# Optimization experiments

Measured on AMD Instinct MI355X. Metric: run time of the kernel, lower is better.

## Reference

```python
import jax, jax.numpy as jnp
import numpy as np

N, E = 50000, 800000
F_IN, F_EMB1, F_EMB2, F_HID, F_OUT = 128, 512, 128, 1024, 64


def _linear_params(k, fan_in, fan_out):
    s = 1.0 / np.sqrt(fan_in)
    kw, kb = jax.random.split(k)
    W = jax.random.uniform(kw, (fan_in, fan_out), jnp.float32, -s, s)
    b = jax.random.uniform(kb, (fan_out,), jnp.float32, -s, s)
    return W, b


def setup_inputs() -> dict:
    key = jax.random.key(0)
    ks = jax.random.split(key, 8)
    x = jax.random.normal(ks[0], (N, F_IN), jnp.float32)
    src = jax.random.randint(ks[1], (E,), 0, N)
    dst = jax.random.randint(ks[2], (E,), 0, N)
    edge_index = jnp.stack([src, dst])  # [2, E]
    edge_weight = jax.random.uniform(ks[3], (E,), jnp.float32)  # positive weights
    W1, b1 = _linear_params(ks[4], F_IN, F_EMB1)
    W2, b2 = _linear_params(ks[5], F_EMB1, F_EMB2)
    W3, b3 = _linear_params(ks[6], F_EMB2, F_HID)
    W4, b4 = _linear_params(ks[7], F_HID, F_OUT)
    return dict(x=x, edge_index=edge_index, edge_weight=edge_weight,
                W1=W1, b1=b1, W2=W2, b2=b2, W3=W3, b3=b3, W4=W4, b4=b4)


def gcn_conv(x, src, dst, w, W, b):
    """PyG GCNConv: transform, then sym-normalized weighted aggregation with self-loops.
    out = D^{-1/2} (A_w + I) D^{-1/2} (x W) + b,  deg = scatter(w @ dst) + 1."""
    n = x.shape[0]
    h = x @ W  # [N, F_out]
    deg = jax.ops.segment_sum(w, dst, num_segments=n) + 1.0  # +1 for self-loop weight
    dinv = jax.lax.rsqrt(deg)
    norm = dinv[src] * w * dinv[dst]  # [E]
    agg = jax.ops.segment_sum(norm[:, None] * h[src], dst, num_segments=n)
    agg = agg + h / deg[:, None]  # self-loop: dinv[i]*1*dinv[i] * h[i]
    return agg + b


def reference(x, edge_index, edge_weight, W1, b1, W2, b2, W3, b3, W4, b4):
    src, dst = edge_index[0], edge_index[1]
    h = jax.nn.relu(gcn_conv(x, src, dst, edge_weight, W1, b1))
    # graph_normalization=False -> identity; dropout is identity in eval mode
    h = jax.nn.relu(gcn_conv(h, src, dst, edge_weight, W2, b2))
    h = jax.nn.relu(h @ W3 + b3)
    out = jax.nn.relu(h @ W4 + b4)
    return out
```

## Files before the change

### kernel.cpp

```cpp
#include <hip/hip_runtime.h>


#define ELLW 64
#define C64S 16

typedef short bf16x8 __attribute__((ext_vector_type(8)));
typedef float f32x4 __attribute__((ext_vector_type(4)));

__device__ __forceinline__ unsigned short f2b(float f) {
    unsigned u = __builtin_bit_cast(unsigned, f);
    unsigned r = (u + 0x7FFFu + ((u >> 16) & 1u)) >> 16;
    return (unsigned short)r;
}
__device__ __forceinline__ float b2f(unsigned short u) {
    return __builtin_bit_cast(float, (unsigned)u << 16);
}

__device__ __forceinline__ void fill_edge(int e, const int* __restrict__ src,
                                          const int* __restrict__ dst,
                                          const float* __restrict__ ew,
                                          unsigned long long* __restrict__ cnt64,
                                          int2* __restrict__ s_edge) {
    int d = dst[e];
    float wv = ew[e];
    unsigned wfix = (unsigned)(wv * 8388608.0f);
    unsigned long long add = ((unsigned long long)1 << 32) | wfix;
    unsigned long long old = atomicAdd(&cnt64[(size_t)d * C64S], add);
    int slot = (int)(old >> 32);
    if (slot < ELLW)
        s_edge[(size_t)d * ELLW + slot] = make_int2(src[e], __builtin_bit_cast(int, wv));
}

__global__ void k_setupA(const float* __restrict__ x,
                         const float* __restrict__ W1, const float* __restrict__ W2,
                         const float* __restrict__ W3, const float* __restrict__ W4,
                         unsigned short* __restrict__ W1t, unsigned short* __restrict__ W2t,
                         unsigned short* __restrict__ W3t, unsigned short* __restrict__ W4t,
                         unsigned short* __restrict__ xb,
                         const int* __restrict__ src, const int* __restrict__ dst,
                         const float* __restrict__ ew,
                         unsigned long long* __restrict__ cnt64,
                         int2* __restrict__ s_edge, int Nn, int E) {
    int b = blockIdx.x;
    if (b < 1563) {
        int e = b * 256 + threadIdx.x;
        int cap = E < 400128 ? E : 400128;
        if (e < cap) fill_edge(e, src, dst, ew, cnt64, s_edge);
    } else if (b < 2843) {
        int i = (b - 1563) * 256 + threadIdx.x;
        if (i < 65536) {
            int k = i >> 9, n = i & 511;
            W1t[n * 128 + k] = f2b(W1[i]);
        } else if (i < 131072) {
            int j = i - 65536; int k = j >> 7, n = j & 127;
            W2t[n * 512 + k] = f2b(W2[j]);
        } else if (i < 262144) {
            int j = i - 131072; int k = j >> 10, n = j & 1023;
            W3t[n * 128 + k] = f2b(W3[j]);
        } else {
            int j = i - 262144; int k = j >> 6, n = j & 63;
            W4t[n * 1024 + k] = f2b(W4[j]);
        }
    } else {
        int i = (b - 2843) * 256 + threadIdx.x;
        if (i < Nn * 32) {
            float4 v = ((const float4*)x)[i];
            ushort4 o;
            o.x = f2b(v.x); o.y = f2b(v.y); o.z = f2b(v.z); o.w = f2b(v.w);
            ((ushort4*)xb)[i] = o;
        }
    }
}

__global__ void k_setupB(const int* __restrict__ src, const int* __restrict__ dst,
                         const float* __restrict__ ew,
                         unsigned long long* __restrict__ cnt64,
                         int2* __restrict__ s_edge, int E) {
    int e = 400128 + blockIdx.x * 256 + (int)threadIdx.x;
    if (e < E) fill_edge(e, src, dst, ew, cnt64, s_edge);
}

__global__ void k_deg(const unsigned long long* __restrict__ cnt64,
                      float* __restrict__ dinv, int Nn) {
    int i = blockIdx.x * 256 + threadIdx.x;
    if (i >= Nn) return;
    unsigned long long cv = cnt64[(size_t)i * C64S];
    float deg = 1.0f + (float)(unsigned)(cv & 0xFFFFFFFFull) * (1.0f / 8388608.0f);
    dinv[i] = rsqrtf(deg);
}

template <bool FIRST, bool BIAS_RELU>
__global__ __launch_bounds__(256) void k_gather(
    const unsigned short* __restrict__ Xb, int2* __restrict__ s_edge,
    const unsigned long long* __restrict__ cnt64, const float* __restrict__ dinv,
    const float* __restrict__ bias, unsigned short* __restrict__ outb, int Nn) {
    int node = blockIdx.x * 4 + (threadIdx.x >> 6);
    if (node >= Nn) return;
    int lane = threadIdx.x & 63;
    float di = dinv[node];
    float dii = di * di;
    ushort2 sv = ((const ushort2*)(Xb + (size_t)node * 128))[lane];
    float ax = b2f(sv.x) * dii, ay = b2f(sv.y) * dii;

    int c = min((int)(cnt64[(size_t)node * C64S] >> 32), ELLW);
    size_t base = (size_t)node * ELLW;
    int sreg = 0;
    float nv = 0.0f;
    if (lane < c) {
        int2 rec = s_edge[base + lane];
        sreg = rec.x;
        if (FIRST) {
            float wv = __builtin_bit_cast(float, rec.y);
            nv = dinv[sreg] * wv * di;
            ((int*)s_edge)[2 * (base + lane) + 1] = __builtin_bit_cast(int, nv);
        } else {
            nv = __builtin_bit_cast(float, rec.y);
        }
    }

    int j = 0;
    for (; j + 8 <= c; j += 8) {
        int s0 = __shfl(sreg, j),     s1 = __shfl(sreg, j + 1);
        int s2 = __shfl(sreg, j + 2), s3 = __shfl(sreg, j + 3);
        int s4 = __shfl(sreg, j + 4), s5 = __shfl(sreg, j + 5);
        int s6 = __shfl(sreg, j + 6), s7 = __shfl(sreg, j + 7);
        float n0 = __shfl(nv, j),     n1 = __shfl(nv, j + 1);
        float n2 = __shfl(nv, j + 2), n3 = __shfl(nv, j + 3);
        float n4 = __shfl(nv, j + 4), n5 = __shfl(nv, j + 5);
        float n6 = __shfl(nv, j + 6), n7 = __shfl(nv, j + 7);
        ushort2 r0 = ((const ushort2*)(Xb + (size_t)s0 * 128))[lane];
        ushort2 r1 = ((const ushort2*)(Xb + (size_t)s1 * 128))[lane];
        ushort2 r2 = ((const ushort2*)(Xb + (size_t)s2 * 128))[lane];
        ushort2 r3 = ((const ushort2*)(Xb + (size_t)s3 * 128))[lane];
        ushort2 r4 = ((const ushort2*)(Xb + (size_t)s4 * 128))[lane];
        ushort2 r5 = ((const ushort2*)(Xb + (size_t)s5 * 128))[lane];
        ushort2 r6 = ((const ushort2*)(Xb + (size_t)s6 * 128))[lane];
        ushort2 r7 = ((const ushort2*)(Xb + (size_t)s7 * 128))[lane];
        ax += n0 * b2f(r0.x) + n1 * b2f(r1.x) + n2 * b2f(r2.x) + n3 * b2f(r3.x);
        ay += n0 * b2f(r0.y) + n1 * b2f(r1.y) + n2 * b2f(r2.y) + n3 * b2f(r3.y);
        ax += n4 * b2f(r4.x) + n5 * b2f(r5.x) + n6 * b2f(r6.x) + n7 * b2f(r7.x);
        ay += n4 * b2f(r4.y) + n5 * b2f(r5.y) + n6 * b2f(r6.y) + n7 * b2f(r7.y);
    }
    for (; j < c; ++j) {
        int sj = __shfl(sreg, j);
        float nj = __shfl(nv, j);
        ushort2 r = ((const ushort2*)(Xb + (size_t)sj * 128))[lane];
        ax += nj * b2f(r.x);
        ay += nj * b2f(r.y);
    }

    if (BIAS_RELU) {
        float2 bv = ((const float2*)bias)[lane];
        ax = fmaxf(ax + bv.x, 0.0f);
        ay = fmaxf(ay + bv.y, 0.0f);
    }
    ushort2 o; o.x = f2b(ax); o.y = f2b(ay);
    ((ushort2*)(outb + (size_t)node * 128))[lane] = o;
}

template <int H, int OUTW, bool HAS_BO, bool OUT_BF16>
__global__ __launch_bounds__(256) void k_mlp(
    const unsigned short* __restrict__ A, const unsigned short* __restrict__ Wht,
    const unsigned short* __restrict__ Wot, const float* __restrict__ bh,
    const float* __restrict__ bo, void* __restrict__ out, int M) {
    constexpr int HC = H / 64;
    constexpr int NJ = OUTW / 16;
    constexpr int OW4 = OUTW / 32;
    __shared__ __align__(16) unsigned short Whs[64 * 128];
    __shared__ __align__(16) unsigned short Ps[128 * 64];
    __shared__ __align__(16) unsigned short Wos[OUTW * 64];
    const int tid = threadIdx.x, wave = tid >> 6, lane = tid & 63;
    const int lm = lane & 15, quad = lane >> 4;
    const int bm0 = blockIdx.x * 128;

    bf16x8 af[2][4];
    #pragma unroll
    for (int i = 0; i < 2; ++i) {
        int gr = bm0 + wave * 32 + i * 16 + lm;
        #pragma unroll
        for (int kb = 0; kb < 4; ++kb) af[i][kb] = bf16x8{0, 0, 0, 0, 0, 0, 0, 0};
        if (gr < M) {
            #pragma unroll
            for (int kb = 0; kb < 4; ++kb)
                af[i][kb] = *(const bf16x8*)(A + (size_t)gr * 128 + kb * 32 + quad * 8);
        }
    }

    #pragma unroll
    for (int u = 0; u < 4; ++u) {
        int idx = tid + u * 256; int r = idx >> 4, g = idx & 15;
        *(int4*)&Whs[r * 128 + ((g ^ (r & 15)) * 8)] =
            *(const int4*)(Wht + (size_t)r * 128 + g * 8);
    }
    #pragma unroll
    for (int u = 0; u < OW4; ++u) {
        int idx = tid + u * 256; int r = idx >> 3, g = idx & 7;
        *(int4*)&Wos[r * 64 + ((g ^ (r & 7)) * 8)] =
            *(const int4*)(Wot + (size_t)r * H + g * 8);
    }
    __syncthreads();

    f32x4 oacc[2][NJ] = {};
    for (int c = 0; c < HC; ++c) {
        f32x4 hacc[2][4] = {};
        #pragma unroll
        for (int kb = 0; kb < 4; ++kb) {
            bf16x8 bfr[4];
            #pragma unroll
            for (int j = 0; j < 4; ++j) {
                int r = j * 16 + lm, g = kb * 4 + quad;
                bfr[j] = *(const bf16x8*)&Whs[r * 128 + ((g ^ (r & 15)) * 8)];
            }
            #pragma unroll
            for (int i = 0; i < 2; ++i)
                #pragma unroll
                for (int j = 0; j < 4; ++j)
                    hacc[i][j] = __builtin_amdgcn_mfma_f32_16x16x32_bf16(
                        af[i][kb], bfr[j], hacc[i][j], 0, 0, 0);
        }

        #pragma unroll
        for (int i = 0; i < 2; ++i) {
            #pragma unroll
            for (int j = 0; j < 4; ++j) {
                int col = j * 16 + lm;
                float bv = bh[c * 64 + col];
                #pragma unroll
                for (int r4 = 0; r4 < 4; ++r4) {
                    int row = wave * 32 + i * 16 + quad * 4 + r4;
                    float o = fmaxf(hacc[i][j][r4] + bv, 0.0f);
                    Ps[row * 64 + (((col >> 3) ^ (row & 7)) * 8) + (col & 7)] = f2b(o);
                }
            }
        }

        #pragma unroll
        for (int kb = 0; kb < 2; ++kb) {
            bf16x8 pf[2];
            #pragma unroll
            for (int i = 0; i < 2; ++i) {
                int r = wave * 32 + i * 16 + lm, g = kb * 4 + quad;
                pf[i] = *(const bf16x8*)&Ps[r * 64 + ((g ^ (r & 7)) * 8)];
            }
            #pragma unroll
            for (int j = 0; j < NJ; ++j) {
                int r = j * 16 + lm, g = kb * 4 + quad;
                bf16x8 wf = *(const bf16x8*)&Wos[r * 64 + ((g ^ (r & 7)) * 8)];
                #pragma unroll
                for (int i = 0; i < 2; ++i)
                    oacc[i][j] = __builtin_amdgcn_mfma_f32_16x16x32_bf16(
                        pf[i], wf, oacc[i][j], 0, 0, 0);
            }
        }

        if (c + 1 < HC) {
            __syncthreads();
            #pragma unroll
            for (int u = 0; u < 4; ++u) {
                int idx = tid + u * 256; int r = idx >> 4, g = idx & 15;
                *(int4*)&Whs[r * 128 + ((g ^ (r & 15)) * 8)] =
                    *(const int4*)(Wht + (size_t)((c + 1) * 64 + r) * 128 + g * 8);
            }
            #pragma unroll
            for (int u = 0; u < OW4; ++u) {
                int idx = tid + u * 256; int r = idx >> 3, g = idx & 7;
                *(int4*)&Wos[r * 64 + ((g ^ (r & 7)) * 8)] =
                    *(const int4*)(Wot + (size_t)r * H + (c + 1) * 64 + g * 8);
            }
            __syncthreads();
        }
    }

    #pragma unroll
    for (int i = 0; i < 2; ++i) {
        #pragma unroll
        for (int j = 0; j < NJ; ++j) {
            int col = j * 16 + lm;
            float bv = HAS_BO ? bo[col] : 0.0f;
            #pragma unroll
            for (int r4 = 0; r4 < 4; ++r4) {
                int m = bm0 + wave * 32 + i * 16 + quad * 4 + r4;
                if (m < M) {
                    float o = oacc[i][j][r4];
                    if (HAS_BO) o = fmaxf(o + bv, 0.0f);
                    if (OUT_BF16)
                        ((unsigned short*)out)[(size_t)m * OUTW + col] = f2b(o);
                    else
                        ((float*)out)[(size_t)m * OUTW + col] = o;
                }
            }
        }
    }
}

static inline int cdiv(long a, long b) { return (int)((a + b - 1) / b); }

extern "C" void kernel_launch(void* const* d_in, const int* in_sizes, int n_in,
                              void* d_out, int out_size, void* d_ws, size_t ws_size,
                              hipStream_t stream) {
    const float* x  = (const float*)d_in[0];
    const int*   ei = (const int*)d_in[1];
    const float* ew = (const float*)d_in[2];
    const float* W1 = (const float*)d_in[3];
    const float* b1 = (const float*)d_in[4];
    const float* W2 = (const float*)d_in[5];
    const float* b2 = (const float*)d_in[6];
    const float* W3 = (const float*)d_in[7];
    const float* b3 = (const float*)d_in[8];
    const float* W4 = (const float*)d_in[9];
    const float* b4 = (const float*)d_in[10];
    const int Nn = in_sizes[0] / 128;
    const int E  = in_sizes[1] / 2;
    const int* src = ei;
    const int* dst = ei + E;

    char* ws = (char*)d_ws;
    size_t off_b = 0;
    auto alloc = [&](size_t bytes) -> void* {
        void* p = ws + off_b;
        off_b += (bytes + 255) & ~(size_t)255;
        return p;
    };
    float*              dinv   = (float*)alloc((size_t)Nn * 4);
    unsigned long long* cnt64  = (unsigned long long*)alloc((size_t)Nn * C64S * 8);
    int2*               s_edge = (int2*)alloc((size_t)Nn * ELLW * 8);
    unsigned short*     W1t    = (unsigned short*)alloc(512 * 128 * 2);
    unsigned short*     W2t    = (unsigned short*)alloc(128 * 512 * 2);
    unsigned short*     W3t    = (unsigned short*)alloc(1024 * 128 * 2);
    unsigned short*     W4t    = (unsigned short*)alloc(64 * 1024 * 2);
    unsigned short*     xb     = (unsigned short*)alloc((size_t)Nn * 128 * 2);
    unsigned short*     t2b    = (unsigned short*)alloc((size_t)Nn * 128 * 2);
    unsigned short*     actb   = (unsigned short*)alloc((size_t)Nn * 128 * 2);
    float*              out    = (float*)d_out;

    hipMemsetAsync(cnt64, 0, (size_t)Nn * C64S * 8, stream);
    k_setupA<<<9093, 256, 0, stream>>>(x, W1, W2, W3, W4, W1t, W2t, W3t, W4t,
                                       xb, src, dst, ew, cnt64, s_edge, Nn, E);
    k_setupB<<<1562, 256, 0, stream>>>(src, dst, ew, cnt64, s_edge, E);
    k_deg<<<cdiv(Nn, 256), 256, 0, stream>>>(cnt64, dinv, Nn);

    k_gather<true, false><<<cdiv(Nn, 4), 256, 0, stream>>>(
        xb, s_edge, cnt64, dinv, nullptr, actb, Nn);
    k_mlp<512, 128, false, true><<<cdiv(Nn, 128), 256, 0, stream>>>(
        actb, W1t, W2t, b1, nullptr, t2b, Nn);

    k_gather<false, true><<<cdiv(Nn, 4), 256, 0, stream>>>(
        t2b, s_edge, cnt64, dinv, b2, actb, Nn);

    k_mlp<1024, 64, true, false><<<cdiv(Nn, 128), 256, 0, stream>>>(
        actb, W3t, W4t, b3, b4, out, Nn);
}
```

Baseline: 284.5 us.

## Double-buffer MLP weight tiles with register prefetch to overlap global loads

The fused MLP kernel now keeps two LDS buffers each for the hidden and output weight chunks. Each iteration loads the next chunk from global memory into registers before the MFMA work, then writes it into the other buffer afterwards. This drops one __syncthreads per chunk and hides global load latency behind compute. In exchange, LDS use roughly doubles for the weight tiles and register pressure rises, which may reduce occupancy.

Result: slower. 377.7 us (+32.8%).

```diff
diff --git a/kernel.cpp b/kernel.cpp
--- a/kernel.cpp
+++ b/kernel.cpp
@@ -166,9 +166,9 @@
     constexpr int HC = H / 64;
     constexpr int NJ = OUTW / 16;
     constexpr int OW4 = OUTW / 32;
-    __shared__ __align__(16) unsigned short Whs[64 * 128];
+    __shared__ __align__(16) unsigned short Whs[2][64 * 128];
     __shared__ __align__(16) unsigned short Ps[128 * 64];
-    __shared__ __align__(16) unsigned short Wos[OUTW * 64];
+    __shared__ __align__(16) unsigned short Wos[2][OUTW * 64];
     const int tid = threadIdx.x, wave = tid >> 6, lane = tid & 63;
     const int lm = lane & 15, quad = lane >> 4;
     const int bm0 = blockIdx.x * 128;
@@ -189,19 +189,36 @@
     #pragma unroll
     for (int u = 0; u < 4; ++u) {
         int idx = tid + u * 256; int r = idx >> 4, g = idx & 15;
-        *(int4*)&Whs[r * 128 + ((g ^ (r & 15)) * 8)] =
+        *(int4*)&Whs[0][r * 128 + ((g ^ (r & 15)) * 8)] =
             *(const int4*)(Wht + (size_t)r * 128 + g * 8);
     }
     #pragma unroll
     for (int u = 0; u < OW4; ++u) {
         int idx = tid + u * 256; int r = idx >> 3, g = idx & 7;
-        *(int4*)&Wos[r * 64 + ((g ^ (r & 7)) * 8)] =
+        *(int4*)&Wos[0][r * 64 + ((g ^ (r & 7)) * 8)] =
             *(const int4*)(Wot + (size_t)r * H + g * 8);
     }
     __syncthreads();
 
     f32x4 oacc[2][NJ] = {};
     for (int c = 0; c < HC; ++c) {
+        const int cur = c & 1;
+        const bool more = (c + 1 < HC);
+
+        int4 pwh[4]; int4 pwo[OW4];
+        if (more) {
+            #pragma unroll
+            for (int u = 0; u < 4; ++u) {
+                int idx = tid + u * 256; int r = idx >> 4, g = idx & 15;
+                pwh[u] = *(const int4*)(Wht + (size_t)((c + 1) * 64 + r) * 128 + g * 8);
+            }
+            #pragma unroll
+            for (int u = 0; u < OW4; ++u) {
+                int idx = tid + u * 256; int r = idx >> 3, g = idx & 7;
+                pwo[u] = *(const int4*)(Wot + (size_t)r * H + (c + 1) * 64 + g * 8);
+            }
+        }
+
         f32x4 hacc[2][4] = {};
         #pragma unroll
         for (int kb = 0; kb < 4; ++kb) {
@@ -209,7 +226,7 @@
             #pragma unroll
             for (int j = 0; j < 4; ++j) {
                 int r = j * 16 + lm, g = kb * 4 + quad;
-                bfr[j] = *(const bf16x8*)&Whs[r * 128 + ((g ^ (r & 15)) * 8)];
+                bfr[j] = *(const bf16x8*)&Whs[cur][r * 128 + ((g ^ (r & 15)) * 8)];
             }
             #pragma unroll
             for (int i = 0; i < 2; ++i)
@@ -245,7 +262,7 @@
             #pragma unroll
             for (int j = 0; j < NJ; ++j) {
                 int r = j * 16 + lm, g = kb * 4 + quad;
-                bf16x8 wf = *(const bf16x8*)&Wos[r * 64 + ((g ^ (r & 7)) * 8)];
+                bf16x8 wf = *(const bf16x8*)&Wos[cur][r * 64 + ((g ^ (r & 7)) * 8)];
                 #pragma unroll
                 for (int i = 0; i < 2; ++i)
                     oacc[i][j] = __builtin_amdgcn_mfma_f32_16x16x32_bf16(
@@ -253,19 +270,16 @@
             }
         }
 
-        if (c + 1 < HC) {
-            __syncthreads();
+        if (more) {
             #pragma unroll
             for (int u = 0; u < 4; ++u) {
                 int idx = tid + u * 256; int r = idx >> 4, g = idx & 15;
-                *(int4*)&Whs[r * 128 + ((g ^ (r & 15)) * 8)] =
-                    *(const int4*)(Wht + (size_t)((c + 1) * 64 + r) * 128 + g * 8);
+                *(int4*)&Whs[cur ^ 1][r * 128 + ((g ^ (r & 15)) * 8)] = pwh[u];
             }
             #pragma unroll
             for (int u = 0; u < OW4; ++u) {
                 int idx = tid + u * 256; int r = idx >> 3, g = idx & 7;
-                *(int4*)&Wos[r * 64 + ((g ^ (r & 7)) * 8)] =
-                    *(const int4*)(Wot + (size_t)r * H + (c + 1) * 64 + g * 8);
+                *(int4*)&Wos[cur ^ 1][r * 64 + ((g ^ (r & 7)) * 8)] = pwo[u];
             }
             __syncthreads();
         }
```
